# Performance work log

Measured on AMD Instinct MI355X. Metric: run time of the kernel, lower is better.

The kernel has to match this reference:

```python
import jax, jax.numpy as jnp
import numpy as np

SCALES = (0.0625, 0.03125, 0.015625)
SIZES = ((14, 25), (7, 13), (4, 7))  # (h, w) feature sizes for 224x398 input
MODEL_H, MODEL_W = 224, 398
SCORE_THRESH = 0.05
IOU_THRESH = 0.6
TOPK = 1000


def _locations(h, w, scale):
    # FCOS grid points at stride 1/scale, centered in each cell; row-major (h, w) flatten
    ys = (jnp.arange(h, dtype=jnp.float32) + 0.5) / scale
    xs = (jnp.arange(w, dtype=jnp.float32) + 0.5) / scale
    Y, X = jnp.meshgrid(ys, xs, indexing='ij')
    return jnp.stack([X.ravel(), Y.ravel()], axis=1)  # (h*w, 2) -> (x, y)


def _decode_level(score_raw, loc_raw, ctr_raw, scale, h, w):
    # score_raw: (1,C,h,w); loc_raw: (1,4,h,w); ctr_raw: (1,1,h,w)
    s = jnp.sqrt(jax.nn.sigmoid(score_raw) * jax.nn.sigmoid(ctr_raw))[0]  # (C,h,w)
    C = s.shape[0]
    s = s.reshape(C, h * w).T                     # (hw, C)
    loc = (loc_raw[0] / scale).reshape(4, h * w).T  # (hw, 4): (l,t,r,b)
    pts = _locations(h, w, scale)
    bbox = jnp.stack([pts[:, 0] - loc[:, 0], pts[:, 1] - loc[:, 1],
                      pts[:, 0] + loc[:, 2], pts[:, 1] + loc[:, 3]], axis=1)
    return s, bbox


def _iou(b):
    area = jnp.maximum(b[:, 2] - b[:, 0], 0.0) * jnp.maximum(b[:, 3] - b[:, 1], 0.0)
    lt = jnp.maximum(b[:, None, :2], b[None, :, :2])
    rb = jnp.minimum(b[:, None, 2:], b[None, :, 2:])
    wh = jnp.maximum(rb - lt, 0.0)
    inter = wh[..., 0] * wh[..., 1]
    return inter / jnp.maximum(area[:, None] + area[None, :] - inter, 1e-9)


def _predict(heads):
    scores, bboxes = [], []
    for (sc_r, lc_r, ct_r), scale, (h, w) in zip(heads, SCALES, SIZES):
        s, b = _decode_level(sc_r, lc_r, ct_r, scale, h, w)
        scores.append(s)
        bboxes.append(b)
    score = jnp.concatenate(scores, 0)[:, 1:]  # drop background column 0
    bbox = jnp.concatenate(bboxes, 0)          # (P, 4)
    nc = score.shape[1]
    flat = score.ravel()                       # (P*nc,)
    masked = jnp.where(flat >= SCORE_THRESH, flat, -1.0)
    top_val, top_idx = jax.lax.top_k(masked, TOPK)  # sorted desc, emulates thresh+topk
    loc_idx = top_idx // nc
    label = top_idx % nc
    bx = bbox[loc_idx]                         # (TOPK, 4)
    valid = top_val >= SCORE_THRESH
    # class-aware NMS via per-class coordinate offsets (torchvision batched_nms)
    off = label.astype(bx.dtype)[:, None] * (jax.lax.stop_gradient(jnp.max(bx)) + 1.0)
    iou = _iou(bx + off)
    idx = jnp.arange(TOPK)

    def body(i, keep):
        sup = keep[i] & (iou[i] > IOU_THRESH) & (idx > i)
        return keep & (~sup)

    keep = jax.lax.fori_loop(0, TOPK, body, valid)
    # clip_boxes_to_image(bbox, size[::-1]) with size=(224,398): torchvision treats
    # (398,224) as (height,width) -> x clipped to [0,224], y clipped to [0,398]
    x1 = jnp.clip(bx[:, 0], 0.0, float(MODEL_H))
    y1 = jnp.clip(bx[:, 1], 0.0, float(MODEL_W))
    x2 = jnp.clip(bx[:, 2], 0.0, float(MODEL_H))
    y2 = jnp.clip(bx[:, 3], 0.0, float(MODEL_W))
    bx = jnp.stack([x1, y1, x2, y2], axis=1)
    # remove_small_boxes(min_size=1e-5)
    keep = keep & ((bx[:, 2] - bx[:, 0]) >= 1e-5) & ((bx[:, 3] - bx[:, 1]) >= 1e-5)
    bx = jnp.where(keep[:, None], bx, 0.0)
    sc = jnp.where(keep, top_val, -1.0)
    return bx, sc, label, keep  # padded to TOPK; keep marks valid detections


def setup_inputs() -> dict:
    key = jax.random.key(0)
    ks = jax.random.split(key, 9)
    C = 81  # class_num + background
    out = {}
    for i, (h, w) in enumerate(SIZES):
        p = f'p{i + 4}'
        out[f'score_{p}'] = jax.random.normal(ks[3 * i], (1, C, h, w), dtype=jnp.float32)
        out[f'loc_{p}'] = jax.random.uniform(ks[3 * i + 1], (1, 4, h, w), dtype=jnp.float32)
        out[f'ctr_{p}'] = jax.random.normal(ks[3 * i + 2], (1, 1, h, w), dtype=jnp.float32)
    return out


def reference(score_p4, loc_p4, ctr_p4, score_p5, loc_p5, ctr_p5,
              score_p6, loc_p6, ctr_p6):
    heads = [(score_p4, loc_p4, ctr_p4),
             (score_p5, loc_p5, ctr_p5),
             (score_p6, loc_p6, ctr_p6)]
    return _predict(heads)
```

## Files before the change

kernel.cpp:

```cpp
#include <hip/hip_runtime.h>
#include <stdint.h>

#define NLOC 469
#define NCLS 80
#define NFLAT 37520
#define TOPK 1000
#define NB 512
#define BOFF 24192
#define CAP 2048

typedef unsigned long long u64;

__device__ __forceinline__ float sigm(float x) { return 1.0f / (1.0f + expf(-x)); }

__device__ __forceinline__ uint32_t f2o(float f) {
    uint32_t u = __float_as_uint(f);
    return (u & 0x80000000u) ? ~u : (u | 0x80000000u);
}

__global__ void decode_kernel(
    const float* __restrict__ s0, const float* __restrict__ l0, const float* __restrict__ c0,
    const float* __restrict__ s1, const float* __restrict__ l1, const float* __restrict__ c1,
    const float* __restrict__ s2, const float* __restrict__ l2, const float* __restrict__ c2,
    u64* __restrict__ keys, float4* __restrict__ bbox, unsigned short* __restrict__ bin16)
{
    int t = blockIdx.x * blockDim.x + threadIdx.x;
    if (t < NFLAT) {
        int p = t / NCLS;
        int k = t - p * NCLS;
        int c = k + 1;
        const float* sr; const float* cr; int local, hw;
        if (p < 350)      { sr = s0; cr = c0; local = p;       hw = 350; }
        else if (p < 441) { sr = s1; cr = c1; local = p - 350; hw = 91;  }
        else              { sr = s2; cr = c2; local = p - 441; hw = 28;  }
        float val = sqrtf(sigm(sr[c * hw + local]) * sigm(cr[local]));
        bool valid = (val >= 0.05f);
        float masked = valid ? val : -1.0f;
        u64 key = ((u64)f2o(masked) << 32) | (u64)(0xFFFFFFFFu - (uint32_t)t);
        keys[t] = key;
        bin16[t] = valid ? (unsigned short)(key >> 49) : (unsigned short)0;
    }
    if (t < NLOC) {
        int p = t;
        const float* lr; int local, hw, w; float is;
        if (p < 350)      { lr = l0; local = p;       hw = 350; w = 25; is = 16.0f; }
        else if (p < 441) { lr = l1; local = p - 350; hw = 91;  w = 13; is = 32.0f; }
        else              { lr = l2; local = p - 441; hw = 28;  w = 7;  is = 64.0f; }
        int y = local / w, x = local - y * w;
        float px = ((float)x + 0.5f) * is;
        float py = ((float)y + 0.5f) * is;
        float L = lr[local] * is;
        float T = lr[hw + local] * is;
        float R = lr[2 * hw + local] * is;
        float B = lr[3 * hw + local] * is;
        bbox[p] = make_float4(px - L, py - T, px + R, py + B);
    }
}

__global__ void __launch_bounds__(1024, 4) topk_kernel(
    const u64* __restrict__ keys, const unsigned short* __restrict__ bin16,
    float* __restrict__ tvalG, int* __restrict__ tidxG)
{
    __shared__ int histW[16 * NB];
    __shared__ int histS[NB];
    __shared__ u64 candL[CAP];
    __shared__ int bstar_s;
    int tid = threadIdx.x;
    int wv = tid >> 6;

    const uint32_t* b2 = (const uint32_t*)bin16;
    const int nw = (tid < 328) ? 19 : 18;
    uint32_t vbuf[19];
    #pragma unroll
    for (int k = 0; k < 19; ++k) {
        int t = tid + (k << 10);
        if (t < NFLAT / 2) vbuf[k] = b2[t];
    }
    if (tid == 0) bstar_s = 0;
    for (int z = tid; z < 16 * NB; z += 1024) histW[z] = 0;
    __syncthreads();
    int* myh = &histW[wv * NB];
    #pragma unroll
    for (int k = 0; k < 19; ++k) {
        if (k < nw) {
            uint32_t v = vbuf[k];
            int b0 = (int)(v & 0xffffu), b1 = (int)(v >> 16);
            if (b0) atomicAdd(&myh[b0 - BOFF], 1);
            if (b1) atomicAdd(&myh[b1 - BOFF], 1);
        }
    }
    __syncthreads();
    if (tid < NB) {
        int s = 0;
        #pragma unroll
        for (int w = 0; w < 16; ++w) s += histW[w * NB + tid];
        histS[tid] = s;
    }
    __syncthreads();
    if (tid < 64) {
        int bs = NB - 8 * (tid + 1);
        int h[8];
        int s = 0;
        #pragma unroll
        for (int k = 0; k < 8; ++k) { h[k] = histS[bs + k]; s += h[k]; }
        int ws = s;
        #pragma unroll
        for (int d = 1; d < 64; d <<= 1) {
            int v = __shfl_up(ws, d, 64);
            if (tid >= d) ws += v;
        }
        int cumAbove = ws - s;
        if (cumAbove < TOPK && ws >= TOPK) {
            int running = cumAbove;
            #pragma unroll
            for (int k = 7; k >= 0; --k) {
                if (running + h[k] >= TOPK) { bstar_s = BOFF + bs + k; break; }
                running += h[k];
            }
        }
        int run = cumAbove;
        #pragma unroll
        for (int k = 7; k >= 0; --k) { histS[bs + k] = run; run += h[k]; }
    }
    __syncthreads();
    int Bstar = bstar_s;
    #pragma unroll
    for (int k = 0; k < 19; ++k) {
        if (k < nw) {
            uint32_t v = vbuf[k];
            int b0 = (int)(v & 0xffffu), b1 = (int)(v >> 16);
            int t2 = (tid + (k << 10)) * 2;
            if (b0 >= Bstar) {
                int pos = atomicAdd(&histS[b0 - BOFF], 1);
                if (pos < CAP) candL[pos] = keys[t2];
            }
            if (b1 >= Bstar) {
                int pos = atomicAdd(&histS[b1 - BOFF], 1);
                if (pos < CAP) candL[pos] = keys[t2 + 1];
            }
        }
    }
    __syncthreads();
    int C = min(histS[Bstar - BOFF], CAP);
    for (int p = tid; p < C; p += 1024) {
        u64 k = candL[p];
        int bidx = (int)(k >> 49) - BOFF;
        int segL = (bidx == NB - 1) ? 0 : min(histS[bidx + 1], CAP);
        int segR = min(histS[bidx], CAP);
        int cnt = segL;
        for (int q = segL; q < segR; ++q)
            cnt += (candL[q] > k) ? 1 : 0;
        if (cnt < TOPK) {
            uint32_t o = (uint32_t)(k >> 32);
            uint32_t u = (o & 0x80000000u) ? (o ^ 0x80000000u) : ~o;
            tvalG[cnt] = __uint_as_float(u);
            tidxG[cnt] = (int)(0xFFFFFFFFu - (uint32_t)(k & 0xFFFFFFFFu));
        }
    }
}

__global__ void __launch_bounds__(1024, 4) nms_kernel(
    const float* __restrict__ tvalG, const int* __restrict__ tidxG,
    const float4* __restrict__ bbox, float* __restrict__ out)
{
    __shared__ uint32_t smask[TOPK * 32];
    __shared__ float4 sboxL[TOPK];
    __shared__ float tvalL[TOPK];
    __shared__ int   tidxL[TOPK];
    __shared__ unsigned char lab8[TOPK];
    __shared__ unsigned char zrow[TOPK];
    __shared__ unsigned short csorted[TOPK];
    __shared__ int clsStart[NCLS], clsCur[NCLS];
    __shared__ uint32_t skeep32[32], validw32[32], zmaskL[32];
    __shared__ float redMax[16], redMin[16];
    __shared__ float Mp1_s;
    __shared__ int dmax_s;

    int tid = threadIdx.x;
    int lane = tid & 63, wv = tid >> 6;

    float tvR = (tid < TOPK) ? tvalG[tid] : -1.0f;
    int   idxR = (tid < TOPK) ? tidxG[tid] : 0;
    int   pR = idxR / NCLS;
    int   labR = idxR - pR * NCLS;
    float4 bR = make_float4(0.f, 0.f, 0.f, 0.f);
    if (tid < TOPK) bR = bbox[pR];

    {
        uint4* z4 = (uint4*)smask;
        for (int z = tid; z < TOPK * 8; z += 1024) z4[z] = make_uint4(0, 0, 0, 0);
    }
    if (tid < TOPK) zrow[tid] = 0;
    float m = -3.0e38f, lmin = 3.0e38f;
    if (tid < TOPK) {
        tvalL[tid] = tvR;
        tidxL[tid] = idxR;
        sboxL[tid] = bR;
        lab8[tid] = (unsigned char)labR;
        m = fmaxf(fmaxf(bR.x, bR.y), fmaxf(bR.z, bR.w));
        lmin = fminf(bR.x, bR.y);
    }
    for (int o = 32; o > 0; o >>= 1) {
        m = fmaxf(m, __shfl_down(m, o, 64));
        lmin = fminf(lmin, __shfl_down(lmin, o, 64));
    }
    if (lane == 0) { redMax[wv] = m; redMin[wv] = lmin; }
    if (tid < NCLS) clsCur[tid] = 0;
    __syncthreads();
    if (tid == 0) {
        float mm = redMax[0], ll = redMin[0];
        for (int q = 1; q < 16; ++q) { mm = fmaxf(mm, redMax[q]); ll = fminf(ll, redMin[q]); }
        float Mp1 = mm + 1.0f;
        Mp1_s = Mp1;
        int dm = 79;
        if (Mp1 > 0.0f) {
            float ratio = (mm - ll) / Mp1;
            dm = (int)ceilf(ratio);
            if (dm < 0) dm = 0;
            if (dm > 79) dm = 79;
        }
        dmax_s = dm;
    }
    __syncthreads();
    float Mp1 = Mp1_s;
    if (tid < TOPK) {
        float off = (float)lab8[tid] * Mp1;
        float4 b = sboxL[tid];
        sboxL[tid] = make_float4(b.x + off, b.y + off, b.z + off, b.w + off);
        atomicAdd(&clsCur[lab8[tid]], 1);
    }
    __syncthreads();
    if (tid < 64) {
        int l = tid;
        int e0 = clsCur[l];
        int e1 = (l < 16) ? clsCur[64 + l] : 0;
        int s = e0;
        for (int d = 1; d < 64; d <<= 1) {
            int v = __shfl_up(s, d, 64);
            if (l >= d) s += v;
        }
        int tot64 = __shfl(s, 63, 64);
        int s2 = e1;
        for (int d = 1; d < 16; d <<= 1) {
            int v = __shfl_up(s2, d, 64);
            if (l >= d) s2 += v;
        }
        int ex0 = s - e0;
        clsStart[l] = ex0;
        clsCur[l] = ex0;
        if (l < 16) {
            int ex1 = tot64 + s2 - e1;
            clsStart[64 + l] = ex1;
            clsCur[64 + l] = ex1;
        }
    }
    __syncthreads();
    if (tid < TOPK) {
        int pos = atomicAdd(&clsCur[lab8[tid]], 1);
        csorted[pos] = (unsigned short)tid;
    }
    __syncthreads();
    if (tid < TOPK) {
        int s = tid;
        int i = csorted[s];
        int c = lab8[i];
        float4 si = sboxL[i];
        float ai = fmaxf(si.z - si.x, 0.f) * fmaxf(si.w - si.y, 0.f);
        int chi = c + dmax_s; if (chi > NCLS - 1) chi = NCLS - 1;
        int endPos = clsCur[chi];
        for (int t = s + 1; t < endPos; ++t) {
            int j = csorted[t];
            float4 sj = sboxL[j];
            float aj = fmaxf(sj.z - sj.x, 0.f) * fmaxf(sj.w - sj.y, 0.f);
            float ltx = fmaxf(si.x, sj.x), lty = fmaxf(si.y, sj.y);
            float rbx = fminf(si.z, sj.z), rby = fminf(si.w, sj.w);
            float iw = fmaxf(rbx - ltx, 0.f), ih = fmaxf(rby - lty, 0.f);
            float inter = iw * ih;
            float iou = inter / fmaxf(ai + aj - inter, 1e-9f);
            if (iou > 0.6f) {
                int lo = min(i, j), hi = max(i, j);
                atomicOr(&smask[lo * 32 + (hi >> 5)], 1u << (hi & 31));
                zrow[lo] = 1;
            }
        }
    }
    __syncthreads();
    {
        u64 zb = __ballot(tid < TOPK && zrow[tid] != 0);
        if (lane == 0) {
            zmaskL[wv * 2]     = (uint32_t)zb;
            zmaskL[wv * 2 + 1] = (uint32_t)(zb >> 32);
        }
        u64 bal = __ballot(tid < TOPK && tvR >= 0.05f);
        if (lane == 0) {
            validw32[wv * 2]     = (uint32_t)bal;
            validw32[wv * 2 + 1] = (uint32_t)(bal >> 32);
        }
    }
    __syncthreads();
    if (tid < 32) {
        const int ln = tid;
        uint32_t vwreg = validw32[ln];
        uint32_t zreg  = zmaskL[ln];
        uint32_t sup = 0;
        for (int wc = 0; wc < 32; ++wc) {
            uint32_t nzw = (uint32_t)__builtin_amdgcn_readlane((int)zreg, wc);
            uint32_t avail = (uint32_t)__builtin_amdgcn_readlane((int)vwreg, wc)
                           & ~(uint32_t)__builtin_amdgcn_readlane((int)sup, wc);
            int p0 = -1, p1 = -1, p2 = -1;
            uint32_t R0 = 0, R1 = 0, R2 = 0;
            if (nzw) { p0 = __ffs(nzw) - 1; nzw &= nzw - 1;
                       R0 = smask[(wc * 32 + p0) * 32 + ln]; }
            if (nzw) { p1 = __ffs(nzw) - 1; nzw &= nzw - 1;
                       R1 = smask[(wc * 32 + p1) * 32 + ln]; }
            if (nzw) { p2 = __ffs(nzw) - 1; nzw &= nzw - 1;
                       R2 = smask[(wc * 32 + p2) * 32 + ln]; }
            while (p0 >= 0) {
                uint32_t rc = (uint32_t)__builtin_amdgcn_readlane((int)R0, wc);
                uint32_t kp = (avail >> p0) & 1u;
                uint32_t mm = 0u - kp;
                sup   |= R0 & mm;
                avail &= ~(rc & mm);
                p0 = p1; R0 = R1; p1 = p2; R1 = R2;
                if (nzw) { p2 = __ffs(nzw) - 1; nzw &= nzw - 1;
                           R2 = smask[(wc * 32 + p2) * 32 + ln]; }
                else p2 = -1;
            }
            if (ln == 0) skeep32[wc] = avail;
        }
    }
    __syncthreads();
    if (tid < TOPK) {
        bool kp = (skeep32[tid >> 5] >> (tid & 31)) & 1u;
        float x1 = fminf(fmaxf(bR.x, 0.f), 224.f);
        float y1 = fminf(fmaxf(bR.y, 0.f), 398.f);
        float x2 = fminf(fmaxf(bR.z, 0.f), 224.f);
        float y2 = fminf(fmaxf(bR.w, 0.f), 398.f);
        kp = kp && ((x2 - x1) >= 1e-5f) && ((y2 - y1) >= 1e-5f);
        out[tid * 4 + 0] = kp ? x1 : 0.f;
        out[tid * 4 + 1] = kp ? y1 : 0.f;
        out[tid * 4 + 2] = kp ? x2 : 0.f;
        out[tid * 4 + 3] = kp ? y2 : 0.f;
        out[4 * TOPK + tid] = kp ? tvR : -1.0f;
        out[5 * TOPK + tid] = (float)labR;
        out[6 * TOPK + tid] = kp ? 1.0f : 0.0f;
    }
}

extern "C" void kernel_launch(void* const* d_in, const int* in_sizes, int n_in,
                              void* d_out, int out_size, void* d_ws, size_t ws_size,
                              hipStream_t stream)
{
    const float* s0 = (const float*)d_in[0];
    const float* l0 = (const float*)d_in[1];
    const float* c0 = (const float*)d_in[2];
    const float* s1 = (const float*)d_in[3];
    const float* l1 = (const float*)d_in[4];
    const float* c1 = (const float*)d_in[5];
    const float* s2 = (const float*)d_in[6];
    const float* l2 = (const float*)d_in[7];
    const float* c2 = (const float*)d_in[8];

    uint8_t* ws = (uint8_t*)d_ws;
    u64*    keys = (u64*)   (ws);
    float4* bbox = (float4*)(ws + 300160);
    unsigned short* bin16 = (unsigned short*)(ws + 307664);
    float*  tvalG = (float*)(ws + 382704);
    int*    tidxG = (int*)  (ws + 386704);

    decode_kernel<<<dim3((NFLAT + 255) / 256), 256, 0, stream>>>(
        s0, l0, c0, s1, l1, c1, s2, l2, c2, keys, bbox, bin16);
    topk_kernel<<<1, 1024, 0, stream>>>(keys, bin16, tvalG, tidxG);
    nms_kernel<<<1, 1024, 0, stream>>>(tvalG, tidxG, bbox, (float*)d_out);
}
```

Measured before the change: 52.16 us.

## Fuse top-k and NMS kernels into one block with shared LDS union

Merges the top-k selection and NMS kernels into a single 1024-thread kernel that passes the top-k results through shared memory instead of global buffers, and reuses one 128KB LDS region for the histogram/candidate arrays and the NMS suppression mask. Decode now writes only a 32-bit ordered score per element; the 64-bit key with index is rebuilt on the fly in the top-k stage, so the separate keys and bin16 buffers are no longer written or read. The intent is to remove one kernel launch and the global-memory traffic between stages. The cost is that each thread now holds 37 loaded words in registers instead of 19, and the large LDS footprint forces one block per CU, though only a single block is launched anyway.

```diff
diff --git a/kernel.cpp b/kernel.cpp
--- a/kernel.cpp
+++ b/kernel.cpp
@@ -22,7 +22,7 @@
     const float* __restrict__ s0, const float* __restrict__ l0, const float* __restrict__ c0,
     const float* __restrict__ s1, const float* __restrict__ l1, const float* __restrict__ c1,
     const float* __restrict__ s2, const float* __restrict__ l2, const float* __restrict__ c2,
-    u64* __restrict__ keys, float4* __restrict__ bbox, unsigned short* __restrict__ bin16)
+    uint32_t* __restrict__ o32, float4* __restrict__ bbox)
 {
     int t = blockIdx.x * blockDim.x + threadIdx.x;
     if (t < NFLAT) {
@@ -35,10 +35,7 @@
         else              { sr = s2; cr = c2; local = p - 441; hw = 28;  }
         float val = sqrtf(sigm(sr[c * hw + local]) * sigm(cr[local]));
         bool valid = (val >= 0.05f);
-        float masked = valid ? val : -1.0f;
-        u64 key = ((u64)f2o(masked) << 32) | (u64)(0xFFFFFFFFu - (uint32_t)t);
-        keys[t] = key;
-        bin16[t] = valid ? (unsigned short)(key >> 49) : (unsigned short)0;
+        o32[t] = valid ? f2o(val) : 0u;
     }
     if (t < NLOC) {
         int p = t;
@@ -57,36 +54,49 @@
     }
 }
 
-__global__ void __launch_bounds__(1024, 4) topk_kernel(
-    const u64* __restrict__ keys, const unsigned short* __restrict__ bin16,
-    float* __restrict__ tvalG, int* __restrict__ tidxG)
+__global__ void __launch_bounds__(1024, 4) fused_kernel(
+    const uint32_t* __restrict__ o32, const float4* __restrict__ bbox,
+    float* __restrict__ out)
 {
-    __shared__ int histW[16 * NB];
-    __shared__ int histS[NB];
-    __shared__ u64 candL[CAP];
+    __shared__ __align__(16) unsigned char ubuf[131072];
+    int*      histW = (int*)ubuf;
+    int*      histS = (int*)(ubuf + 65536);
+    u64*      candL = (u64*)(ubuf + 69632);
+    uint32_t* smask = (uint32_t*)ubuf;
+
+    __shared__ float4 sboxL[TOPK];
+    __shared__ float tvalL[TOPK];
+    __shared__ int   tidxL[TOPK];
+    __shared__ unsigned char lab8[TOPK];
+    __shared__ unsigned char zrow[TOPK];
+    __shared__ unsigned short csorted[TOPK];
+    __shared__ int clsStart[NCLS], clsCur[NCLS];
+    __shared__ uint32_t skeep32[32], validw32[32], zmaskL[32];
+    __shared__ float redMax[16], redMin[16];
+    __shared__ float Mp1_s;
+    __shared__ int dmax_s;
     __shared__ int bstar_s;
+
     int tid = threadIdx.x;
-    int wv = tid >> 6;
-
-    const uint32_t* b2 = (const uint32_t*)bin16;
-    const int nw = (tid < 328) ? 19 : 18;
-    uint32_t vbuf[19];
+    int lane = tid & 63, wv = tid >> 6;
+
+    const int nw = (tid < 656) ? 37 : 36;
+    uint32_t vbuf[37];
     #pragma unroll
-    for (int k = 0; k < 19; ++k) {
+    for (int k = 0; k < 37; ++k) {
         int t = tid + (k << 10);
-        if (t < NFLAT / 2) vbuf[k] = b2[t];
+        if (t < NFLAT) vbuf[k] = o32[t];
     }
     if (tid == 0) bstar_s = 0;
+    if (tid < TOPK) { tvalL[tid] = -1.0f; tidxL[tid] = 0; }
     for (int z = tid; z < 16 * NB; z += 1024) histW[z] = 0;
     __syncthreads();
     int* myh = &histW[wv * NB];
     #pragma unroll
-    for (int k = 0; k < 19; ++k) {
+    for (int k = 0; k < 37; ++k) {
         if (k < nw) {
-            uint32_t v = vbuf[k];
-            int b0 = (int)(v & 0xffffu), b1 = (int)(v >> 16);
-            if (b0) atomicAdd(&myh[b0 - BOFF], 1);
-            if (b1) atomicAdd(&myh[b1 - BOFF], 1);
+            uint32_t o = vbuf[k];
+            if (o) atomicAdd(&myh[(o >> 17) - BOFF], 1);
         }
     }
     __syncthreads();
@@ -125,62 +135,39 @@
     __syncthreads();
     int Bstar = bstar_s;
     #pragma unroll
-    for (int k = 0; k < 19; ++k) {
+    for (int k = 0; k < 37; ++k) {
         if (k < nw) {
-            uint32_t v = vbuf[k];
-            int b0 = (int)(v & 0xffffu), b1 = (int)(v >> 16);
-            int t2 = (tid + (k << 10)) * 2;
-            if (b0 >= Bstar) {
-                int pos = atomicAdd(&histS[b0 - BOFF], 1);
-                if (pos < CAP) candL[pos] = keys[t2];
-            }
-            if (b1 >= Bstar) {
-                int pos = atomicAdd(&histS[b1 - BOFF], 1);
-                if (pos < CAP) candL[pos] = keys[t2 + 1];
+            uint32_t o = vbuf[k];
+            int b = (int)(o >> 17);
+            if (o && b >= Bstar) {
+                int t = tid + (k << 10);
+                int pos = atomicAdd(&histS[b - BOFF], 1);
+                if (pos < CAP)
+                    candL[pos] = ((u64)o << 32) | (u64)(0xFFFFFFFFu - (uint32_t)t);
             }
         }
     }
     __syncthreads();
     int C = min(histS[Bstar - BOFF], CAP);
     for (int p = tid; p < C; p += 1024) {
-        u64 k = candL[p];
-        int bidx = (int)(k >> 49) - BOFF;
+        u64 kk = candL[p];
+        int bidx = (int)(kk >> 49) - BOFF;
         int segL = (bidx == NB - 1) ? 0 : min(histS[bidx + 1], CAP);
         int segR = min(histS[bidx], CAP);
         int cnt = segL;
         for (int q = segL; q < segR; ++q)
-            cnt += (candL[q] > k) ? 1 : 0;
+            cnt += (candL[q] > kk) ? 1 : 0;
         if (cnt < TOPK) {
-            uint32_t o = (uint32_t)(k >> 32);
+            uint32_t o = (uint32_t)(kk >> 32);
             uint32_t u = (o & 0x80000000u) ? (o ^ 0x80000000u) : ~o;
-            tvalG[cnt] = __uint_as_float(u);
-            tidxG[cnt] = (int)(0xFFFFFFFFu - (uint32_t)(k & 0xFFFFFFFFu));
-        }
-    }
-}
-
-__global__ void __launch_bounds__(1024, 4) nms_kernel(
-    const float* __restrict__ tvalG, const int* __restrict__ tidxG,
-    const float4* __restrict__ bbox, float* __restrict__ out)
-{
-    __shared__ uint32_t smask[TOPK * 32];
-    __shared__ float4 sboxL[TOPK];
-    __shared__ float tvalL[TOPK];
-    __shared__ int   tidxL[TOPK];
-    __shared__ unsigned char lab8[TOPK];
-    __shared__ unsigned char zrow[TOPK];
-    __shared__ unsigned short csorted[TOPK];
-    __shared__ int clsStart[NCLS], clsCur[NCLS];
-    __shared__ uint32_t skeep32[32], validw32[32], zmaskL[32];
-    __shared__ float redMax[16], redMin[16];
-    __shared__ float Mp1_s;
-    __shared__ int dmax_s;
-
-    int tid = threadIdx.x;
-    int lane = tid & 63, wv = tid >> 6;
-
-    float tvR = (tid < TOPK) ? tvalG[tid] : -1.0f;
-    int   idxR = (tid < TOPK) ? tidxG[tid] : 0;
+            tvalL[cnt] = __uint_as_float(u);
+            tidxL[cnt] = (int)(0xFFFFFFFFu - (uint32_t)(kk & 0xFFFFFFFFu));
+        }
+    }
+    __syncthreads();
+
+    float tvR = (tid < TOPK) ? tvalL[tid] : -1.0f;
+    int   idxR = (tid < TOPK) ? tidxL[tid] : 0;
     int   pR = idxR / NCLS;
     int   labR = idxR - pR * NCLS;
     float4 bR = make_float4(0.f, 0.f, 0.f, 0.f);
@@ -193,8 +180,6 @@
     if (tid < TOPK) zrow[tid] = 0;
     float m = -3.0e38f, lmin = 3.0e38f;
     if (tid < TOPK) {
-        tvalL[tid] = tvR;
-        tidxL[tid] = idxR;
         sboxL[tid] = bR;
         lab8[tid] = (unsigned char)labR;
         m = fmaxf(fmaxf(bR.x, bR.y), fmaxf(bR.z, bR.w));
@@ -224,10 +209,9 @@
     __syncthreads();
     float Mp1 = Mp1_s;
     if (tid < TOPK) {
-        float off = (float)lab8[tid] * Mp1;
-        float4 b = sboxL[tid];
-        sboxL[tid] = make_float4(b.x + off, b.y + off, b.z + off, b.w + off);
-        atomicAdd(&clsCur[lab8[tid]], 1);
+        float off = (float)labR * Mp1;
+        sboxL[tid] = make_float4(bR.x + off, bR.y + off, bR.z + off, bR.w + off);
+        atomicAdd(&clsCur[labR], 1);
     }
     __syncthreads();
     if (tid < 64) {
@@ -256,7 +240,7 @@
     }
     __syncthreads();
     if (tid < TOPK) {
-        int pos = atomicAdd(&clsCur[lab8[tid]], 1);
+        int pos = atomicAdd(&clsCur[labR], 1);
         csorted[pos] = (unsigned short)tid;
     }
     __syncthreads();
@@ -362,14 +346,10 @@
     const float* c2 = (const float*)d_in[8];
 
     uint8_t* ws = (uint8_t*)d_ws;
-    u64*    keys = (u64*)   (ws);
-    float4* bbox = (float4*)(ws + 300160);
-    unsigned short* bin16 = (unsigned short*)(ws + 307664);
-    float*  tvalG = (float*)(ws + 382704);
-    int*    tidxG = (int*)  (ws + 386704);
+    uint32_t* o32  = (uint32_t*)(ws);
+    float4*   bbox = (float4*)  (ws + 150080);
 
     decode_kernel<<<dim3((NFLAT + 255) / 256), 256, 0, stream>>>(
-        s0, l0, c0, s1, l1, c1, s2, l2, c2, keys, bbox, bin16);
-    topk_kernel<<<1, 1024, 0, stream>>>(keys, bin16, tvalG, tidxG);
-    nms_kernel<<<1, 1024, 0, stream>>>(tvalG, tidxG, bbox, (float*)d_out);
+        s0, l0, c0, s1, l1, c1, s2, l2, c2, o32, bbox);
+    fused_kernel<<<1, 1024, 0, stream>>>(o32, bbox, (float*)d_out);
 }
```

New measurement: 46.20 us (median of 2 runs). -11.4%, faster.
